# Optimization experiments

Hardware: AMD Instinct MI355X
Metric: run time of the kernel (lower is better)

The kernel has to match this reference:

```python
import jax, jax.numpy as jnp
import numpy as np

EPS = 1e-5
N_NODES = 50000


def batchnorm(x, gamma, beta):
    # training-mode BatchNorm1d: batch mean, biased variance
    mean = jnp.mean(x, axis=0)
    var = jnp.mean(jnp.square(x - mean), axis=0)
    return (x - mean) * jax.lax.rsqrt(var + EPS) * gamma + beta


def setup_inputs() -> dict:
    key = jax.random.key(0)
    ks = jax.random.split(key, 8)
    N, E, D_IN, D_H, D_OUT = N_NODES, 800000, 128, 128, 128
    feat = jax.random.normal(ks[0], (N, D_IN), dtype=jnp.float32)
    w = jax.random.uniform(ks[1], (E,), dtype=jnp.float32)
    # xavier_uniform with relu gain for Q and W
    gain = float(np.sqrt(2.0))
    bq = gain * np.sqrt(6.0 / (D_IN + D_H))
    bw = gain * np.sqrt(6.0 / (D_IN + D_H + D_OUT))
    Q_w = jax.random.uniform(ks[2], (D_H, D_IN), minval=-bq, maxval=bq, dtype=jnp.float32)
    W_w = jax.random.uniform(ks[3], (D_OUT, D_IN + D_H), minval=-bw, maxval=bw, dtype=jnp.float32)
    Q_b = jnp.zeros((D_H,), jnp.float32)
    W_b = jnp.zeros((D_OUT,), jnp.float32)
    gamma2 = jnp.ones((D_OUT,), jnp.float32)
    beta2 = jnp.zeros((D_OUT,), jnp.float32)
    src = jax.random.randint(ks[4], (E,), 0, N, dtype=jnp.int32)
    dst = jax.random.randint(ks[5], (E,), 0, N, dtype=jnp.int32)
    return {"feat": feat, "w": w, "Q_w": Q_w, "Q_b": Q_b, "W_w": W_w,
            "W_b": W_b, "gamma2": gamma2, "beta2": beta2, "src": src, "dst": dst}


def reference(feat, w, Q_w, Q_b, W_w, W_b, gamma2, beta2, src, dst):
    N = feat.shape[0]
    # h = dropout(bnorm_two(relu(Q(feat))))  (dropout=0 -> identity; source reuses bnorm_two)
    h = batchnorm(jax.nn.relu(feat @ Q_w.T + Q_b), gamma2, beta2)  # [N, H]
    # weighted neighbor mean: sum_e w_e * h[src_e] scattered to dst, / sum_e w_e
    num = jax.ops.segment_sum(w[:, None] * h[src], dst, num_segments=N)  # [N, H]
    den = jax.ops.segment_sum(w, dst, num_segments=N)  # [N]
    has_msg = den[:, None] != 0
    agg = jnp.where(has_msg, num / jnp.where(has_msg, den[:, None], 1.0), h)
    rst = jnp.concatenate([feat, agg], axis=1) @ W_w.T + W_b  # [N, OUT]
    rst = batchnorm(jax.nn.relu(rst), gamma2, beta2)
    denom = jnp.linalg.norm(rst, axis=1, keepdims=True)
    return rst / jnp.where(denom == 0, 1.0, denom)
```

## Files before the change

### kernel.cpp

```cpp
#include <hip/hip_runtime.h>
#include <stdint.h>


#define BN_EPS 1e-5f
#define NSLOT 32

typedef __attribute__((ext_vector_type(8))) short bf16x8;
typedef __attribute__((ext_vector_type(4))) float f32x4;

static __device__ __forceinline__ unsigned short f2bf(float f) {
    uint32_t u = __builtin_bit_cast(uint32_t, f);
    u += 0x7fffu + ((u >> 16) & 1u);
    return (unsigned short)(u >> 16);
}
static __device__ __forceinline__ float bf_lo(uint32_t u) {
    return __builtin_bit_cast(float, u << 16);
}
static __device__ __forceinline__ float bf_hi(uint32_t u) {
    return __builtin_bit_cast(float, u & 0xffff0000u);
}

static __device__ __forceinline__ void cast_blk(
    const float* __restrict__ src, unsigned short* __restrict__ dst,
    int n, int blk)
{
    int i = (blk * 256 + threadIdx.x) * 4;
    if (i + 3 < n) {
        float4 v = *(const float4*)(src + i);
        ushort4 o;
        o.x = f2bf(v.x); o.y = f2bf(v.y); o.z = f2bf(v.z); o.w = f2bf(v.w);
        *(ushort4*)(dst + i) = o;
    } else {
        for (int j = i; j < n; ++j) dst[j] = f2bf(src[j]);
    }
}

__global__ __launch_bounds__(256) void k_pre(
    const float* __restrict__ feat, unsigned short* __restrict__ featb, int nf,
    const int* __restrict__ dst, int* __restrict__ ccnt, int E, int CB, int HB,
    const float* __restrict__ Qw, unsigned short* __restrict__ Qwb,
    const float* __restrict__ Ww, unsigned short* __restrict__ Wwb)
{
    int b = (int)blockIdx.x;
    if (b < CB) { cast_blk(feat, featb, nf, b); return; }
    b -= CB;
    if (b >= HB) {
        b -= HB;
        if (b < 16) cast_blk(Qw, Qwb, 128 * 128, b);
        else        cast_blk(Ww, Wwb, 128 * 256, b - 16);
        return;
    }
    __shared__ int hcnt[128];
    const int tid = threadIdx.x;
    if (tid < 128) hcnt[tid] = 0;
    __syncthreads();
    const int base_e = b * 2048;
#pragma unroll
    for (int j = 0; j < 8; ++j) {
        int e = base_e + j * 256 + tid;
        if (e < E) atomicAdd(&hcnt[dst[e] >> 9], 1);
    }
    __syncthreads();
    if (tid < 128 && hcnt[tid] > 0) atomicAdd(&ccnt[tid], hcnt[tid]);
}

__global__ __launch_bounds__(128) void k_coffs(
    const int* __restrict__ ccnt, int* __restrict__ coffs,
    int* __restrict__ gcur, int* __restrict__ offs, int N, int E)
{
    __shared__ int w0sum;
    const int t = threadIdx.x;
    const int lane = t & 63, wv = t >> 6;
    int v = ccnt[t];
    int incl = v;
#pragma unroll
    for (int o = 1; o < 64; o <<= 1) {
        int u = __shfl_up(incl, o, 64);
        if (lane >= o) incl += u;
    }
    if (wv == 0 && lane == 63) w0sum = incl;
    __syncthreads();
    int excl = incl - v + (wv ? w0sum : 0);
    coffs[t] = excl;
    gcur[t]  = excl;
    if (t == 127) { coffs[128] = excl + v; offs[N] = E; }
}

template<int K, bool OUT_BF16>
static __device__ __forceinline__ void gemm_body(
    int bid,
    const unsigned short* __restrict__ A_lo,
    const unsigned short* __restrict__ A_hi,
    const unsigned short* __restrict__ Bb,
    const float* __restrict__ bias,
    void* __restrict__ Yv,
    double* __restrict__ sum, double* __restrict__ sumsq, int N)
{
    constexpr int SA = 72;
    __shared__ unsigned short As[64 * SA];
    __shared__ unsigned short Bs[128 * SA];
    __shared__ float bsum_s[128], bsq_s[128];

    const int tid  = threadIdx.x;
    const int lane = tid & 63;
    const int wv   = tid >> 6;
    const int wr   = wv >> 1;
    const int wc   = wv & 1;
    const int m15  = lane & 15;
    const int quad = lane >> 4;
    const int r0   = bid * 64;

    if (tid < 128) { bsum_s[tid] = 0.f; bsq_s[tid] = 0.f; }

    f32x4 acc[2][4];
#pragma unroll
    for (int rt = 0; rt < 2; ++rt)
#pragma unroll
        for (int ct = 0; ct < 4; ++ct)
            acc[rt][ct] = (f32x4){0.f, 0.f, 0.f, 0.f};

    for (int kc = 0; kc < K; kc += 64) {
        const unsigned short* Ap = (kc < 128) ? A_lo : A_hi;
        const int koff = kc & 127;
#pragma unroll
        for (int i = 0; i < 2; ++i) {
            int idx = i * 256 + tid;
            int row = idx >> 3, seg = idx & 7;
            int gr  = r0 + row; if (gr >= N) gr = N - 1;
            uint4 v = *(const uint4*)(Ap + (size_t)gr * 128 + koff + seg * 8);
            *(uint4*)(As + row * SA + seg * 8) = v;
        }
#pragma unroll
        for (int i = 0; i < 4; ++i) {
            int idx = i * 256 + tid;
            int row = idx >> 3, seg = idx & 7;
            uint4 v = *(const uint4*)(Bb + (size_t)row * K + kc + seg * 8);
            *(uint4*)(Bs + row * SA + seg * 8) = v;
        }
        __syncthreads();

#pragma unroll
        for (int ks = 0; ks < 64; ks += 32) {
            bf16x8 af[2], bfr[4];
#pragma unroll
            for (int rt = 0; rt < 2; ++rt)
                af[rt] = *(const bf16x8*)(As + (wr * 32 + rt * 16 + m15) * SA + ks + quad * 8);
#pragma unroll
            for (int ct = 0; ct < 4; ++ct)
                bfr[ct] = *(const bf16x8*)(Bs + (wc * 64 + ct * 16 + m15) * SA + ks + quad * 8);
#pragma unroll
            for (int rt = 0; rt < 2; ++rt)
#pragma unroll
                for (int ct = 0; ct < 4; ++ct)
                    acc[rt][ct] = __builtin_amdgcn_mfma_f32_16x16x32_bf16(
                        af[rt], bfr[ct], acc[rt][ct], 0, 0, 0);
        }
        __syncthreads();
    }

#pragma unroll
    for (int ct = 0; ct < 4; ++ct) {
        int col = wc * 64 + ct * 16 + m15;
        float bz = bias[col];
        float s = 0.f, q = 0.f;
#pragma unroll
        for (int rt = 0; rt < 2; ++rt) {
#pragma unroll
            for (int reg = 0; reg < 4; ++reg) {
                int row = r0 + wr * 32 + rt * 16 + quad * 4 + reg;
                float vv = fmaxf(acc[rt][ct][reg] + bz, 0.f);
                if (row < N) {
                    if constexpr (OUT_BF16)
                        ((unsigned short*)Yv)[(size_t)row * 128 + col] = f2bf(vv);
                    else
                        ((float*)Yv)[(size_t)row * 128 + col] = vv;
                } else {
                    vv = 0.f;
                }
                s += vv; q = fmaf(vv, vv, q);
            }
        }
        s += __shfl_xor(s, 16, 64); s += __shfl_xor(s, 32, 64);
        q += __shfl_xor(q, 16, 64); q += __shfl_xor(q, 32, 64);
        if (quad == 0) {
            atomicAdd(&bsum_s[col], s);
            atomicAdd(&bsq_s[col], q);
        }
    }
    __syncthreads();
    if (tid < 128) {
        const int slot = (bid & (NSLOT - 1)) * 128;
        atomicAdd(&sum[slot + tid],   (double)bsum_s[tid]);
        atomicAdd(&sumsq[slot + tid], (double)bsq_s[tid]);
    }
}

static __device__ __forceinline__ void bn_coef_body(
    int t, const double* __restrict__ sum, const double* __restrict__ sumsq,
    const float* __restrict__ gamma, const float* __restrict__ beta,
    float* __restrict__ a, float* __restrict__ b, double invN)
{
    double ms = 0.0, qs = 0.0;
#pragma unroll
    for (int s = 0; s < NSLOT; ++s) {
        ms += sum[s * 128 + t];
        qs += sumsq[s * 128 + t];
    }
    float mean = (float)(ms * invN);
    float var  = (float)(qs * invN) - mean * mean;
    float sc = rsqrtf(var + BN_EPS) * gamma[t];
    a[t] = sc;
    b[t] = fmaf(-mean, sc, beta[t]);
}

__global__ __launch_bounds__(128) void bn_coef(
    const double* __restrict__ sum, const double* __restrict__ sumsq,
    const float* __restrict__ gamma, const float* __restrict__ beta,
    float* __restrict__ a, float* __restrict__ b, double invN)
{
    bn_coef_body(threadIdx.x, sum, sumsq, gamma, beta, a, b, invN);
}

static __device__ __forceinline__ void bin_body(
    int bid,
    const int* __restrict__ src, const int* __restrict__ dst,
    const float* __restrict__ w, int* __restrict__ gcur,
    int4* __restrict__ tmp, int E)
{
    __shared__ int hcnt[128];
    __shared__ int hbase[128];
    const int tid = threadIdx.x;
    if (tid < 128) hcnt[tid] = 0;
    __syncthreads();

    int d8[8], s8[8], slot8[8];
    float w8[8];
#pragma unroll
    for (int j = 0; j < 8; ++j) {
        int e = bid * 2048 + j * 256 + tid;
        if (e < E) {
            d8[j] = dst[e]; s8[j] = src[e]; w8[j] = w[e];
            slot8[j] = atomicAdd(&hcnt[d8[j] >> 9], 1);
        } else d8[j] = -1;
    }
    __syncthreads();
    if (tid < 128 && hcnt[tid] > 0)
        hbase[tid] = atomicAdd(&gcur[tid], hcnt[tid]);
    __syncthreads();
#pragma unroll
    for (int j = 0; j < 8; ++j) {
        if (d8[j] >= 0) {
            int pos = hbase[d8[j] >> 9] + slot8[j];
            tmp[pos] = make_int4(s8[j], __float_as_int(w8[j]), d8[j], 0);
        }
    }
}

__global__ __launch_bounds__(256) void k_bin_gemm(
    const int* __restrict__ src, const int* __restrict__ dst,
    const float* __restrict__ w, int* __restrict__ gcur,
    int4* __restrict__ tmp, int E, int HB,
    const unsigned short* __restrict__ featb,
    const unsigned short* __restrict__ Qwb, const float* __restrict__ Qb,
    unsigned short* __restrict__ y1b,
    double* __restrict__ sum, double* __restrict__ sumsq, int N)
{
    if ((int)blockIdx.x < HB)
        bin_body(blockIdx.x, src, dst, w, gcur, tmp, E);
    else
        gemm_body<128, true>(blockIdx.x - HB, featb, featb, Qwb, Qb, y1b,
                             sum, sumsq, N);
}

static __device__ __forceinline__ void refine_body(
    int b,
    const int4* __restrict__ tmp, const int* __restrict__ coffs,
    int* __restrict__ offs, int2* __restrict__ epack, int N)
{
    __shared__ int hist[512];
    __shared__ int wpre[4];
    const int d0   = b << 9;
    const int dlim = min(512, N - d0);
    const int tid  = threadIdx.x;
    const int lane = tid & 63, wv = tid >> 6;
    const int start = coffs[b];
    const int end   = coffs[b + 1];

    hist[tid] = 0; hist[tid + 256] = 0;
    __syncthreads();

    for (int p = start + tid; p < end; p += 256)
        atomicAdd(&hist[tmp[p].z - d0], 1);
    __syncthreads();

    int v0 = hist[2 * tid], v1 = hist[2 * tid + 1];
    int s = v0 + v1;
    int incl = s;
#pragma unroll
    for (int o = 1; o < 64; o <<= 1) {
        int t = __shfl_up(incl, o, 64);
        if (lane >= o) incl += t;
    }
    if (lane == 63) wpre[wv] = incl;
    __syncthreads();
    if (tid == 0) {
        int r = 0;
#pragma unroll
        for (int i = 0; i < 4; ++i) { int t = wpre[i]; wpre[i] = r; r += t; }
    }
    __syncthreads();
    int e0 = start + wpre[wv] + incl - s;
    if (2 * tid < dlim)     offs[d0 + 2 * tid]     = e0;
    if (2 * tid + 1 < dlim) offs[d0 + 2 * tid + 1] = e0 + v0;
    hist[2 * tid]     = e0;
    hist[2 * tid + 1] = e0 + v0;
    __syncthreads();

    for (int p = start + tid; p < end; p += 256) {
        int4 rec = tmp[p];
        int pos = atomicAdd(&hist[rec.z - d0], 1);
        epack[pos] = make_int2(rec.x, rec.y);
    }
}

__global__ __launch_bounds__(256) void k_bnref(
    const double* __restrict__ sum, const double* __restrict__ sumsq,
    const float* __restrict__ gamma, const float* __restrict__ beta,
    float* __restrict__ a, float* __restrict__ b, double invN,
    const int4* __restrict__ tmp, const int* __restrict__ coffs,
    int* __restrict__ offs, int2* __restrict__ epack, int N)
{
    if (blockIdx.x == 0) {
        if (threadIdx.x < 128)
            bn_coef_body(threadIdx.x, sum, sumsq, gamma, beta, a, b, invN);
        return;
    }
    refine_body((int)blockIdx.x - 1, tmp, coffs, offs, epack, N);
}

__global__ __launch_bounds__(256) void gather_agg(
    const unsigned short* __restrict__ y1b,
    const int* __restrict__ offs, const int2* __restrict__ epack,
    const float* __restrict__ a, const float* __restrict__ b,
    unsigned short* __restrict__ aggb, int N)
{
    const int r    = (int)((blockIdx.x * 256u + threadIdx.x) >> 6);
    const int lane = threadIdx.x & 63;
    const int li   = lane & 31;
    const int hf   = lane >> 5;
    if (r >= N) return;
    int p = offs[r];
    const int end = offs[r + 1];
    float ac0 = 0.f, ac1 = 0.f, ac2 = 0.f, ac3 = 0.f, den = 0.f;
    for (; p + 3 < end; p += 4) {
        int2 ea = epack[p + hf];
        int2 eb = epack[p + 2 + hf];
        uint2 ua = *(const uint2*)(y1b + (size_t)ea.x * 128 + 4 * li);
        uint2 ub = *(const uint2*)(y1b + (size_t)eb.x * 128 + 4 * li);
        float wa = __int_as_float(ea.y), wb = __int_as_float(eb.y);
        ac0 = fmaf(wa, bf_lo(ua.x), ac0); ac1 = fmaf(wa, bf_hi(ua.x), ac1);
        ac2 = fmaf(wa, bf_lo(ua.y), ac2); ac3 = fmaf(wa, bf_hi(ua.y), ac3);
        ac0 = fmaf(wb, bf_lo(ub.x), ac0); ac1 = fmaf(wb, bf_hi(ub.x), ac1);
        ac2 = fmaf(wb, bf_lo(ub.y), ac2); ac3 = fmaf(wb, bf_hi(ub.y), ac3);
        den += wa + wb;
    }
    for (; p + 1 < end; p += 2) {
        int2 ea = epack[p + hf];
        uint2 ua = *(const uint2*)(y1b + (size_t)ea.x * 128 + 4 * li);
        float wa = __int_as_float(ea.y);
        ac0 = fmaf(wa, bf_lo(ua.x), ac0); ac1 = fmaf(wa, bf_hi(ua.x), ac1);
        ac2 = fmaf(wa, bf_lo(ua.y), ac2); ac3 = fmaf(wa, bf_hi(ua.y), ac3);
        den += wa;
    }
    if (p < end && hf == 0) {
        int2 ea = epack[p];
        uint2 ua = *(const uint2*)(y1b + (size_t)ea.x * 128 + 4 * li);
        float wa = __int_as_float(ea.y);
        ac0 = fmaf(wa, bf_lo(ua.x), ac0); ac1 = fmaf(wa, bf_hi(ua.x), ac1);
        ac2 = fmaf(wa, bf_lo(ua.y), ac2); ac3 = fmaf(wa, bf_hi(ua.y), ac3);
        den += wa;
    }
    ac0 += __shfl_xor(ac0, 32, 64);
    ac1 += __shfl_xor(ac1, 32, 64);
    ac2 += __shfl_xor(ac2, 32, 64);
    ac3 += __shfl_xor(ac3, 32, 64);
    den += __shfl_xor(den, 32, 64);
    if (hf) return;
    const int c = 4 * li;
    float4 av = *(const float4*)(a + c);
    float4 bv = *(const float4*)(b + c);
    float m0, m1, m2, m3;
    if (den != 0.f) {
        float inv = 1.f / den;
        m0 = ac0 * inv; m1 = ac1 * inv; m2 = ac2 * inv; m3 = ac3 * inv;
    } else {
        uint2 u = *(const uint2*)(y1b + (size_t)r * 128 + c);
        m0 = bf_lo(u.x); m1 = bf_hi(u.x); m2 = bf_lo(u.y); m3 = bf_hi(u.y);
    }
    ushort4 o;
    o.x = f2bf(fmaf(av.x, m0, bv.x));
    o.y = f2bf(fmaf(av.y, m1, bv.y));
    o.z = f2bf(fmaf(av.z, m2, bv.z));
    o.w = f2bf(fmaf(av.w, m3, bv.w));
    *(ushort4*)(aggb + (size_t)r * 128 + c) = o;
}

__global__ __launch_bounds__(256) void gemm_bn2(
    const unsigned short* __restrict__ A_lo,
    const unsigned short* __restrict__ A_hi,
    const unsigned short* __restrict__ Bb,
    const float* __restrict__ bias,
    float* __restrict__ Y,
    double* __restrict__ sum, double* __restrict__ sumsq, int N)
{
    gemm_body<256, false>(blockIdx.x, A_lo, A_hi, Bb, bias, Y, sum, sumsq, N);
}

__global__ __launch_bounds__(256) void finalize(
    const float* __restrict__ Y2,
    const float* __restrict__ a, const float* __restrict__ b,
    float* __restrict__ out, int N)
{
    __shared__ float sa[128], sb[128];
    const int t = threadIdx.x;
    if (t < 128) { sa[t] = a[t]; sb[t] = b[t]; }
    __syncthreads();
    const int row  = (int)((blockIdx.x * 256u + t) >> 6);
    const int lane = t & 63;
    if (row >= N) return;
    const size_t base = (size_t)row * 128;
    float v0 = fmaf(sa[lane],      Y2[base + lane],      sb[lane]);
    float v1 = fmaf(sa[lane + 64], Y2[base + lane + 64], sb[lane + 64]);
    float ss = fmaf(v0, v0, v1 * v1);
#pragma unroll
    for (int o = 32; o; o >>= 1) ss += __shfl_xor(ss, o, 64);
    float nrm = sqrtf(ss);
    float inv = (nrm == 0.f) ? 1.f : 1.f / nrm;
    out[base + lane]      = v0 * inv;
    out[base + lane + 64] = v1 * inv;
}

extern "C" void kernel_launch(void* const* d_in, const int* in_sizes, int n_in,
                              void* d_out, int out_size, void* d_ws, size_t ws_size,
                              hipStream_t stream)
{
    const float* feat   = (const float*)d_in[0];
    const float* w      = (const float*)d_in[1];
    const float* Q_w    = (const float*)d_in[2];
    const float* Q_b    = (const float*)d_in[3];
    const float* W_w    = (const float*)d_in[4];
    const float* W_b    = (const float*)d_in[5];
    const float* gamma2 = (const float*)d_in[6];
    const float* beta2  = (const float*)d_in[7];
    const int*   src    = (const int*)d_in[8];
    const int*   dst    = (const int*)d_in[9];

    const int N = in_sizes[0] / 128;
    const int E = in_sizes[1];

    float*          y2    = (float*)d_ws;
    unsigned short* featb = (unsigned short*)(y2 + (size_t)N * 128);
    unsigned short* aggb  = featb + (size_t)N * 128;
    unsigned short* y1b   = aggb + (size_t)N * 128;
    int4*  tmp    = (int4*)(y1b + (size_t)N * 128);
    int2*  epack  = (int2*)(tmp + E);
    int*   offs   = (int*)(epack + E);
    int*   coffs  = offs + (N + 1);
    int*   gcur   = coffs + 129;
    float* coefs  = (float*)(gcur + 128);
    float* a1 = coefs, *b1 = coefs + 128, *a2 = coefs + 256, *b2 = coefs + 384;
    uintptr_t qp = ((uintptr_t)(coefs + 512) + 15) & ~(uintptr_t)15;
    unsigned short* Qwb = (unsigned short*)qp;
    unsigned short* Wwb = Qwb + 128 * 128;
    uintptr_t sp = ((uintptr_t)(Wwb + 128 * 256) + 15) & ~(uintptr_t)15;
    double* stats = (double*)sp;
    double* sum1   = stats;
    double* sumsq1 = stats + NSLOT * 128;
    double* sum2   = stats + 2 * NSLOT * 128;
    double* sumsq2 = stats + 3 * NSLOT * 128;
    int*   ccnt   = (int*)(stats + 4 * NSLOT * 128);

    hipMemsetAsync(stats, 0,
                   4 * NSLOT * 128 * sizeof(double) + 128 * sizeof(int),
                   stream);

    const double invN = 1.0 / (double)N;
    const int GB = (N + 63) / 64;
    const int NB = (N + 511) >> 9;
    const int CB = (N * 128 / 4 + 255) / 256;
    const int HB = (E + 2047) / 2048;
    const int QB = 16;
    const int WB = 32;

    k_pre<<<CB + HB + QB + WB, 256, 0, stream>>>(
        feat, featb, N * 128, dst, ccnt, E, CB, HB,
        Q_w, Qwb, W_w, Wwb);
    k_coffs<<<1, 128, 0, stream>>>(ccnt, coffs, gcur, offs, N, E);

    k_bin_gemm<<<HB + GB, 256, 0, stream>>>(
        src, dst, w, gcur, tmp, E, HB,
        featb, Qwb, Q_b, y1b, sum1, sumsq1, N);

    k_bnref<<<NB + 1, 256, 0, stream>>>(
        sum1, sumsq1, gamma2, beta2, a1, b1, invN,
        tmp, coffs, offs, epack, N);

    gather_agg<<<(N * 64 + 255) / 256, 256, 0, stream>>>(
        y1b, offs, epack, a1, b1, aggb, N);

    gemm_bn2<<<GB, 256, 0, stream>>>(
        featb, aggb, Wwb, W_b, y2, sum2, sumsq2, N);
    bn_coef<<<1, 128, 0, stream>>>(sum2, sumsq2, gamma2, beta2, a2, b2, invN);
    finalize<<<(N * 64 + 255) / 256, 256, 0, stream>>>(
        y2, a2, b2, (float*)d_out, N);
}
```

Before: 227.7 us.

## Fuse neighbor gather-aggregation into second GEMM prologue via shared memory

The separate gather_agg kernel is removed. The second GEMM block now computes the weighted neighbor mean and batchnorm affine for its 64 rows directly into shared memory, then uses that tile as the upper K half of the A operand. This avoids writing and re-reading the bf16 agg buffer and saves one kernel launch. In exchange, the gather now runs at the lower parallelism of the GEMM grid (one block per 64 rows, one wave per row at a time, serialized over 16 iterations), which can reduce latency hiding for the random gathers.

```diff
diff --git a/kernel.cpp b/kernel.cpp
--- a/kernel.cpp
+++ b/kernel.cpp
@@ -86,14 +86,12 @@
     if (t == 127) { coffs[128] = excl + v; offs[N] = E; }
 }
 
-template<int K, bool OUT_BF16>
-static __device__ __forceinline__ void gemm_body(
+static __device__ __forceinline__ void gemm1_body(
     int bid,
-    const unsigned short* __restrict__ A_lo,
-    const unsigned short* __restrict__ A_hi,
+    const unsigned short* __restrict__ A,
     const unsigned short* __restrict__ Bb,
     const float* __restrict__ bias,
-    void* __restrict__ Yv,
+    unsigned short* __restrict__ Y,
     double* __restrict__ sum, double* __restrict__ sumsq, int N)
 {
     constexpr int SA = 72;
@@ -119,22 +117,20 @@
         for (int ct = 0; ct < 4; ++ct)
             acc[rt][ct] = (f32x4){0.f, 0.f, 0.f, 0.f};
 
-    for (int kc = 0; kc < K; kc += 64) {
-        const unsigned short* Ap = (kc < 128) ? A_lo : A_hi;
-        const int koff = kc & 127;
+    for (int kc = 0; kc < 128; kc += 64) {
 #pragma unroll
         for (int i = 0; i < 2; ++i) {
             int idx = i * 256 + tid;
             int row = idx >> 3, seg = idx & 7;
             int gr  = r0 + row; if (gr >= N) gr = N - 1;
-            uint4 v = *(const uint4*)(Ap + (size_t)gr * 128 + koff + seg * 8);
+            uint4 v = *(const uint4*)(A + (size_t)gr * 128 + kc + seg * 8);
             *(uint4*)(As + row * SA + seg * 8) = v;
         }
 #pragma unroll
         for (int i = 0; i < 4; ++i) {
             int idx = i * 256 + tid;
             int row = idx >> 3, seg = idx & 7;
-            uint4 v = *(const uint4*)(Bb + (size_t)row * K + kc + seg * 8);
+            uint4 v = *(const uint4*)(Bb + (size_t)row * 128 + kc + seg * 8);
             *(uint4*)(Bs + row * SA + seg * 8) = v;
         }
         __syncthreads();
@@ -170,10 +166,7 @@
                 int row = r0 + wr * 32 + rt * 16 + quad * 4 + reg;
                 float vv = fmaxf(acc[rt][ct][reg] + bz, 0.f);
                 if (row < N) {
-                    if constexpr (OUT_BF16)
-                        ((unsigned short*)Yv)[(size_t)row * 128 + col] = f2bf(vv);
-                    else
-                        ((float*)Yv)[(size_t)row * 128 + col] = vv;
+                    Y[(size_t)row * 128 + col] = f2bf(vv);
                 } else {
                     vv = 0.f;
                 }
@@ -268,8 +261,7 @@
     if ((int)blockIdx.x < HB)
         bin_body(blockIdx.x, src, dst, w, gcur, tmp, E);
     else
-        gemm_body<128, true>(blockIdx.x - HB, featb, featb, Qwb, Qb, y1b,
-                             sum, sumsq, N);
+        gemm1_body(blockIdx.x - HB, featb, Qwb, Qb, y1b, sum, sumsq, N);
 }
 
 static __device__ __forceinline__ void refine_body(
@@ -338,82 +330,178 @@
     refine_body((int)blockIdx.x - 1, tmp, coffs, offs, epack, N);
 }
 
-__global__ __launch_bounds__(256) void gather_agg(
+__global__ __launch_bounds__(256) void gemm2_fused(
+    const unsigned short* __restrict__ featb,
     const unsigned short* __restrict__ y1b,
     const int* __restrict__ offs, const int2* __restrict__ epack,
-    const float* __restrict__ a, const float* __restrict__ b,
-    unsigned short* __restrict__ aggb, int N)
-{
-    const int r    = (int)((blockIdx.x * 256u + threadIdx.x) >> 6);
-    const int lane = threadIdx.x & 63;
-    const int li   = lane & 31;
-    const int hf   = lane >> 5;
-    if (r >= N) return;
-    int p = offs[r];
-    const int end = offs[r + 1];
-    float ac0 = 0.f, ac1 = 0.f, ac2 = 0.f, ac3 = 0.f, den = 0.f;
-    for (; p + 3 < end; p += 4) {
-        int2 ea = epack[p + hf];
-        int2 eb = epack[p + 2 + hf];
-        uint2 ua = *(const uint2*)(y1b + (size_t)ea.x * 128 + 4 * li);
-        uint2 ub = *(const uint2*)(y1b + (size_t)eb.x * 128 + 4 * li);
-        float wa = __int_as_float(ea.y), wb = __int_as_float(eb.y);
-        ac0 = fmaf(wa, bf_lo(ua.x), ac0); ac1 = fmaf(wa, bf_hi(ua.x), ac1);
-        ac2 = fmaf(wa, bf_lo(ua.y), ac2); ac3 = fmaf(wa, bf_hi(ua.y), ac3);
-        ac0 = fmaf(wb, bf_lo(ub.x), ac0); ac1 = fmaf(wb, bf_hi(ub.x), ac1);
-        ac2 = fmaf(wb, bf_lo(ub.y), ac2); ac3 = fmaf(wb, bf_hi(ub.y), ac3);
-        den += wa + wb;
-    }
-    for (; p + 1 < end; p += 2) {
-        int2 ea = epack[p + hf];
-        uint2 ua = *(const uint2*)(y1b + (size_t)ea.x * 128 + 4 * li);
-        float wa = __int_as_float(ea.y);
-        ac0 = fmaf(wa, bf_lo(ua.x), ac0); ac1 = fmaf(wa, bf_hi(ua.x), ac1);
-        ac2 = fmaf(wa, bf_lo(ua.y), ac2); ac3 = fmaf(wa, bf_hi(ua.y), ac3);
-        den += wa;
-    }
-    if (p < end && hf == 0) {
-        int2 ea = epack[p];
-        uint2 ua = *(const uint2*)(y1b + (size_t)ea.x * 128 + 4 * li);
-        float wa = __int_as_float(ea.y);
-        ac0 = fmaf(wa, bf_lo(ua.x), ac0); ac1 = fmaf(wa, bf_hi(ua.x), ac1);
-        ac2 = fmaf(wa, bf_lo(ua.y), ac2); ac3 = fmaf(wa, bf_hi(ua.y), ac3);
-        den += wa;
-    }
-    ac0 += __shfl_xor(ac0, 32, 64);
-    ac1 += __shfl_xor(ac1, 32, 64);
-    ac2 += __shfl_xor(ac2, 32, 64);
-    ac3 += __shfl_xor(ac3, 32, 64);
-    den += __shfl_xor(den, 32, 64);
-    if (hf) return;
-    const int c = 4 * li;
-    float4 av = *(const float4*)(a + c);
-    float4 bv = *(const float4*)(b + c);
-    float m0, m1, m2, m3;
-    if (den != 0.f) {
-        float inv = 1.f / den;
-        m0 = ac0 * inv; m1 = ac1 * inv; m2 = ac2 * inv; m3 = ac3 * inv;
-    } else {
-        uint2 u = *(const uint2*)(y1b + (size_t)r * 128 + c);
-        m0 = bf_lo(u.x); m1 = bf_hi(u.x); m2 = bf_lo(u.y); m3 = bf_hi(u.y);
-    }
-    ushort4 o;
-    o.x = f2bf(fmaf(av.x, m0, bv.x));
-    o.y = f2bf(fmaf(av.y, m1, bv.y));
-    o.z = f2bf(fmaf(av.z, m2, bv.z));
-    o.w = f2bf(fmaf(av.w, m3, bv.w));
-    *(ushort4*)(aggb + (size_t)r * 128 + c) = o;
-}
-
-__global__ __launch_bounds__(256) void gemm_bn2(
-    const unsigned short* __restrict__ A_lo,
-    const unsigned short* __restrict__ A_hi,
+    const float* __restrict__ a1, const float* __restrict__ b1,
     const unsigned short* __restrict__ Bb,
     const float* __restrict__ bias,
     float* __restrict__ Y,
     double* __restrict__ sum, double* __restrict__ sumsq, int N)
 {
-    gemm_body<256, false>(blockIdx.x, A_lo, A_hi, Bb, bias, Y, sum, sumsq, N);
+    constexpr int SA = 72;
+    __shared__ unsigned short As[64 * SA];
+    __shared__ unsigned short Bs[128 * SA];
+    __shared__ unsigned short Ag[2][64 * SA];
+    __shared__ float bsum_s[128], bsq_s[128];
+
+    const int tid  = threadIdx.x;
+    const int lane = tid & 63;
+    const int wv   = tid >> 6;
+    const int wr   = wv >> 1;
+    const int wc   = wv & 1;
+    const int m15  = lane & 15;
+    const int quad = lane >> 4;
+    const int r0   = (int)blockIdx.x * 64;
+
+    if (tid < 128) { bsum_s[tid] = 0.f; bsq_s[tid] = 0.f; }
+
+    const int li = lane & 31;
+    const int hf = lane >> 5;
+    const int c  = 4 * li;
+    const float4 av = *(const float4*)(a1 + c);
+    const float4 bv = *(const float4*)(b1 + c);
+#pragma unroll 1
+    for (int i = 0; i < 16; ++i) {
+        const int lr = wv + 4 * i;
+        const int r  = r0 + lr;
+        float ac0 = 0.f, ac1 = 0.f, ac2 = 0.f, ac3 = 0.f, den = 0.f;
+        if (r < N) {
+            int p = offs[r];
+            const int end = offs[r + 1];
+            for (; p + 3 < end; p += 4) {
+                int2 ea = epack[p + hf];
+                int2 eb = epack[p + 2 + hf];
+                uint2 ua = *(const uint2*)(y1b + (size_t)ea.x * 128 + c);
+                uint2 ub = *(const uint2*)(y1b + (size_t)eb.x * 128 + c);
+                float wa = __int_as_float(ea.y), wb = __int_as_float(eb.y);
+                ac0 = fmaf(wa, bf_lo(ua.x), ac0); ac1 = fmaf(wa, bf_hi(ua.x), ac1);
+                ac2 = fmaf(wa, bf_lo(ua.y), ac2); ac3 = fmaf(wa, bf_hi(ua.y), ac3);
+                ac0 = fmaf(wb, bf_lo(ub.x), ac0); ac1 = fmaf(wb, bf_hi(ub.x), ac1);
+                ac2 = fmaf(wb, bf_lo(ub.y), ac2); ac3 = fmaf(wb, bf_hi(ub.y), ac3);
+                den += wa + wb;
+            }
+            for (; p + 1 < end; p += 2) {
+                int2 ea = epack[p + hf];
+                uint2 ua = *(const uint2*)(y1b + (size_t)ea.x * 128 + c);
+                float wa = __int_as_float(ea.y);
+                ac0 = fmaf(wa, bf_lo(ua.x), ac0); ac1 = fmaf(wa, bf_hi(ua.x), ac1);
+                ac2 = fmaf(wa, bf_lo(ua.y), ac2); ac3 = fmaf(wa, bf_hi(ua.y), ac3);
+                den += wa;
+            }
+            if (p < end && hf == 0) {
+                int2 ea = epack[p];
+                uint2 ua = *(const uint2*)(y1b + (size_t)ea.x * 128 + c);
+                float wa = __int_as_float(ea.y);
+                ac0 = fmaf(wa, bf_lo(ua.x), ac0); ac1 = fmaf(wa, bf_hi(ua.x), ac1);
+                ac2 = fmaf(wa, bf_lo(ua.y), ac2); ac3 = fmaf(wa, bf_hi(ua.y), ac3);
+                den += wa;
+            }
+        }
+        ac0 += __shfl_xor(ac0, 32, 64);
+        ac1 += __shfl_xor(ac1, 32, 64);
+        ac2 += __shfl_xor(ac2, 32, 64);
+        ac3 += __shfl_xor(ac3, 32, 64);
+        den += __shfl_xor(den, 32, 64);
+        if (hf == 0) {
+            float m0 = 0.f, m1 = 0.f, m2 = 0.f, m3 = 0.f;
+            if (den != 0.f) {
+                float inv = 1.f / den;
+                m0 = ac0 * inv; m1 = ac1 * inv; m2 = ac2 * inv; m3 = ac3 * inv;
+            } else if (r < N) {
+                uint2 u = *(const uint2*)(y1b + (size_t)r * 128 + c);
+                m0 = bf_lo(u.x); m1 = bf_hi(u.x); m2 = bf_lo(u.y); m3 = bf_hi(u.y);
+            }
+            ushort4 o;
+            o.x = f2bf(fmaf(av.x, m0, bv.x));
+            o.y = f2bf(fmaf(av.y, m1, bv.y));
+            o.z = f2bf(fmaf(av.z, m2, bv.z));
+            o.w = f2bf(fmaf(av.w, m3, bv.w));
+            *(ushort4*)(Ag[li >> 4] + lr * SA + (c & 63)) = o;
+        }
+    }
+    __syncthreads();
+
+    f32x4 acc[2][4];
+#pragma unroll
+    for (int rt = 0; rt < 2; ++rt)
+#pragma unroll
+        for (int ct = 0; ct < 4; ++ct)
+            acc[rt][ct] = (f32x4){0.f, 0.f, 0.f, 0.f};
+
+    for (int kc = 0; kc < 256; kc += 64) {
+        if (kc < 128) {
+#pragma unroll
+            for (int i = 0; i < 2; ++i) {
+                int idx = i * 256 + tid;
+                int row = idx >> 3, seg = idx & 7;
+                int gr  = r0 + row; if (gr >= N) gr = N - 1;
+                uint4 v = *(const uint4*)(featb + (size_t)gr * 128 + kc + seg * 8);
+                *(uint4*)(As + row * SA + seg * 8) = v;
+            }
+        }
+#pragma unroll
+        for (int i = 0; i < 4; ++i) {
+            int idx = i * 256 + tid;
+            int row = idx >> 3, seg = idx & 7;
+            uint4 v = *(const uint4*)(Bb + (size_t)row * 256 + kc + seg * 8);
+            *(uint4*)(Bs + row * SA + seg * 8) = v;
+        }
+        __syncthreads();
+
+        const unsigned short* Ap = (kc < 128) ? As : Ag[(kc >> 6) & 1];
+#pragma unroll
+        for (int ks = 0; ks < 64; ks += 32) {
+            bf16x8 af[2], bfr[4];
+#pragma unroll
+            for (int rt = 0; rt < 2; ++rt)
+                af[rt] = *(const bf16x8*)(Ap + (wr * 32 + rt * 16 + m15) * SA + ks + quad * 8);
+#pragma unroll
+            for (int ct = 0; ct < 4; ++ct)
+                bfr[ct] = *(const bf16x8*)(Bs + (wc * 64 + ct * 16 + m15) * SA + ks + quad * 8);
+#pragma unroll
+            for (int rt = 0; rt < 2; ++rt)
+#pragma unroll
+                for (int ct = 0; ct < 4; ++ct)
+                    acc[rt][ct] = __builtin_amdgcn_mfma_f32_16x16x32_bf16(
+                        af[rt], bfr[ct], acc[rt][ct], 0, 0, 0);
+        }
+        __syncthreads();
+    }
+
+#pragma unroll
+    for (int ct = 0; ct < 4; ++ct) {
+        int col = wc * 64 + ct * 16 + m15;
+        float bz = bias[col];
+        float s = 0.f, q = 0.f;
+#pragma unroll
+        for (int rt = 0; rt < 2; ++rt) {
+#pragma unroll
+            for (int reg = 0; reg < 4; ++reg) {
+                int row = r0 + wr * 32 + rt * 16 + quad * 4 + reg;
+                float vv = fmaxf(acc[rt][ct][reg] + bz, 0.f);
+                if (row < N) {
+                    Y[(size_t)row * 128 + col] = vv;
+                } else {
+                    vv = 0.f;
+                }
+                s += vv; q = fmaf(vv, vv, q);
+            }
+        }
+        s += __shfl_xor(s, 16, 64); s += __shfl_xor(s, 32, 64);
+        q += __shfl_xor(q, 16, 64); q += __shfl_xor(q, 32, 64);
+        if (quad == 0) {
+            atomicAdd(&bsum_s[col], s);
+            atomicAdd(&bsq_s[col], q);
+        }
+    }
+    __syncthreads();
+    if (tid < 128) {
+        const int slot = ((int)blockIdx.x & (NSLOT - 1)) * 128;
+        atomicAdd(&sum[slot + tid],   (double)bsum_s[tid]);
+        atomicAdd(&sumsq[slot + tid], (double)bsq_s[tid]);
+    }
 }
 
 __global__ __launch_bounds__(256) void finalize(
@@ -460,8 +548,7 @@
 
     float*          y2    = (float*)d_ws;
     unsigned short* featb = (unsigned short*)(y2 + (size_t)N * 128);
-    unsigned short* aggb  = featb + (size_t)N * 128;
-    unsigned short* y1b   = aggb + (size_t)N * 128;
+    unsigned short* y1b   = featb + (size_t)N * 128;
     int4*  tmp    = (int4*)(y1b + (size_t)N * 128);
     int2*  epack  = (int2*)(tmp + E);
     int*   offs   = (int*)(epack + E);
@@ -505,11 +592,10 @@
         sum1, sumsq1, gamma2, beta2, a1, b1, invN,
         tmp, coffs, offs, epack, N);
 
-    gather_agg<<<(N * 64 + 255) / 256, 256, 0, stream>>>(
-        y1b, offs, epack, a1, b1, aggb, N);
-
-    gemm_bn2<<<GB, 256, 0, stream>>>(
-        featb, aggb, Wwb, W_b, y2, sum2, sumsq2, N);
+    gemm2_fused<<<GB, 256, 0, stream>>>(
+        featb, y1b, offs, epack, a1, b1, Wwb, W_b,
+        y2, sum2, sumsq2, N);
+
     bn_coef<<<1, 128, 0, stream>>>(sum2, sumsq2, gamma2, beta2, a2, b2, invN);
     finalize<<<(N * 64 + 255) / 256, 256, 0, stream>>>(
         y2, a2, b2, (float*)d_out, N);
```

Result: slower. 300.6 us (+32.0%).

## Remove coarse-offset scan kernel by recomputing scan in consumers; unroll gather by 8

Applied to the files above, without the earlier changes.

Drops the single-block k_coffs launch. The bin and refine blocks now each redo the 128-entry prefix scan of the bucket counts, and bin blocks add the scanned base to a zero-initialised per-bucket cursor. The offs[N] sentinel write moves into k_pre. Separately, the gather loop gains an 8-edge unrolled step to keep more independent row loads in flight. The cost is a redundant small scan in every bin and refine block, plus more registers in the gather.

```diff
diff --git a/kernel.cpp b/kernel.cpp
--- a/kernel.cpp
+++ b/kernel.cpp
@@ -35,14 +35,42 @@
     }
 }
 
+static __device__ __forceinline__ void scan_ccnt(
+    const int* __restrict__ ccnt, int* excl_out, int* v_out, int* w0s)
+{
+    const int t = threadIdx.x;
+    int v = 0, incl = 0;
+    if (t < 128) {
+        v = ccnt[t];
+        incl = v;
+        const int lane = t & 63;
+#pragma unroll
+        for (int o = 1; o < 64; o <<= 1) {
+            int u = __shfl_up(incl, o, 64);
+            if (lane >= o) incl += u;
+        }
+        if (t == 63) *w0s = incl;
+    }
+    __syncthreads();
+    int excl = 0;
+    if (t < 128) excl = incl - v + ((t >> 6) ? *w0s : 0);
+    *excl_out = excl;
+    *v_out = v;
+}
+
 __global__ __launch_bounds__(256) void k_pre(
     const float* __restrict__ feat, unsigned short* __restrict__ featb, int nf,
     const int* __restrict__ dst, int* __restrict__ ccnt, int E, int CB, int HB,
     const float* __restrict__ Qw, unsigned short* __restrict__ Qwb,
-    const float* __restrict__ Ww, unsigned short* __restrict__ Wwb)
+    const float* __restrict__ Ww, unsigned short* __restrict__ Wwb,
+    int* __restrict__ offs, int N)
 {
     int b = (int)blockIdx.x;
-    if (b < CB) { cast_blk(feat, featb, nf, b); return; }
+    if (b < CB) {
+        if (b == 0 && threadIdx.x == 0) offs[N] = E;
+        cast_blk(feat, featb, nf, b);
+        return;
+    }
     b -= CB;
     if (b >= HB) {
         b -= HB;
@@ -62,28 +90,6 @@
     }
     __syncthreads();
     if (tid < 128 && hcnt[tid] > 0) atomicAdd(&ccnt[tid], hcnt[tid]);
-}
-
-__global__ __launch_bounds__(128) void k_coffs(
-    const int* __restrict__ ccnt, int* __restrict__ coffs,
-    int* __restrict__ gcur, int* __restrict__ offs, int N, int E)
-{
-    __shared__ int w0sum;
-    const int t = threadIdx.x;
-    const int lane = t & 63, wv = t >> 6;
-    int v = ccnt[t];
-    int incl = v;
-#pragma unroll
-    for (int o = 1; o < 64; o <<= 1) {
-        int u = __shfl_up(incl, o, 64);
-        if (lane >= o) incl += u;
-    }
-    if (wv == 0 && lane == 63) w0sum = incl;
-    __syncthreads();
-    int excl = incl - v + (wv ? w0sum : 0);
-    coffs[t] = excl;
-    gcur[t]  = excl;
-    if (t == 127) { coffs[128] = excl + v; offs[N] = E; }
 }
 
 template<int K, bool OUT_BF16>
@@ -224,11 +230,13 @@
 static __device__ __forceinline__ void bin_body(
     int bid,
     const int* __restrict__ src, const int* __restrict__ dst,
-    const float* __restrict__ w, int* __restrict__ gcur,
+    const float* __restrict__ w,
+    const int* __restrict__ ccnt, int* __restrict__ gofs,
     int4* __restrict__ tmp, int E)
 {
     __shared__ int hcnt[128];
     __shared__ int hbase[128];
+    __shared__ int w0s;
     const int tid = threadIdx.x;
     if (tid < 128) hcnt[tid] = 0;
     __syncthreads();
@@ -244,8 +252,10 @@
         } else d8[j] = -1;
     }
     __syncthreads();
+    int excl, vcnt;
+    scan_ccnt(ccnt, &excl, &vcnt, &w0s);
     if (tid < 128 && hcnt[tid] > 0)
-        hbase[tid] = atomicAdd(&gcur[tid], hcnt[tid]);
+        hbase[tid] = excl + atomicAdd(&gofs[tid], hcnt[tid]);
     __syncthreads();
 #pragma unroll
     for (int j = 0; j < 8; ++j) {
@@ -258,7 +268,8 @@
 
 __global__ __launch_bounds__(256) void k_bin_gemm(
     const int* __restrict__ src, const int* __restrict__ dst,
-    const float* __restrict__ w, int* __restrict__ gcur,
+    const float* __restrict__ w,
+    const int* __restrict__ ccnt, int* __restrict__ gofs,
     int4* __restrict__ tmp, int E, int HB,
     const unsigned short* __restrict__ featb,
     const unsigned short* __restrict__ Qwb, const float* __restrict__ Qb,
@@ -266,7 +277,7 @@
     double* __restrict__ sum, double* __restrict__ sumsq, int N)
 {
     if ((int)blockIdx.x < HB)
-        bin_body(blockIdx.x, src, dst, w, gcur, tmp, E);
+        bin_body(blockIdx.x, src, dst, w, ccnt, gofs, tmp, E);
     else
         gemm_body<128, true>(blockIdx.x - HB, featb, featb, Qwb, Qb, y1b,
                              sum, sumsq, N);
@@ -274,20 +285,26 @@
 
 static __device__ __forceinline__ void refine_body(
     int b,
-    const int4* __restrict__ tmp, const int* __restrict__ coffs,
+    const int4* __restrict__ tmp, const int* __restrict__ ccnt,
     int* __restrict__ offs, int2* __restrict__ epack, int N)
 {
     __shared__ int hist[512];
     __shared__ int wpre[4];
+    __shared__ int w0s;
+    __shared__ int sbounds[2];
     const int d0   = b << 9;
     const int dlim = min(512, N - d0);
     const int tid  = threadIdx.x;
     const int lane = tid & 63, wv = tid >> 6;
-    const int start = coffs[b];
-    const int end   = coffs[b + 1];
 
     hist[tid] = 0; hist[tid + 256] = 0;
     __syncthreads();
+    int excl, vcnt;
+    scan_ccnt(ccnt, &excl, &vcnt, &w0s);
+    if (tid == b) { sbounds[0] = excl; sbounds[1] = excl + vcnt; }
+    __syncthreads();
+    const int start = sbounds[0];
+    const int end   = sbounds[1];
 
     for (int p = start + tid; p < end; p += 256)
         atomicAdd(&hist[tmp[p].z - d0], 1);
@@ -327,7 +344,7 @@
     const double* __restrict__ sum, const double* __restrict__ sumsq,
     const float* __restrict__ gamma, const float* __restrict__ beta,
     float* __restrict__ a, float* __restrict__ b, double invN,
-    const int4* __restrict__ tmp, const int* __restrict__ coffs,
+    const int4* __restrict__ tmp, const int* __restrict__ ccnt,
     int* __restrict__ offs, int2* __restrict__ epack, int N)
 {
     if (blockIdx.x == 0) {
@@ -335,7 +352,7 @@
             bn_coef_body(threadIdx.x, sum, sumsq, gamma, beta, a, b, invN);
         return;
     }
-    refine_body((int)blockIdx.x - 1, tmp, coffs, offs, epack, N);
+    refine_body((int)blockIdx.x - 1, tmp, ccnt, offs, epack, N);
 }
 
 __global__ __launch_bounds__(256) void gather_agg(
@@ -351,12 +368,34 @@
     if (r >= N) return;
     int p = offs[r];
     const int end = offs[r + 1];
+    const int c = 4 * li;
     float ac0 = 0.f, ac1 = 0.f, ac2 = 0.f, ac3 = 0.f, den = 0.f;
+    for (; p + 7 < end; p += 8) {
+        int2 e0 = epack[p + hf];
+        int2 e1 = epack[p + 2 + hf];
+        int2 e2 = epack[p + 4 + hf];
+        int2 e3 = epack[p + 6 + hf];
+        uint2 u0 = *(const uint2*)(y1b + (size_t)e0.x * 128 + c);
+        uint2 u1 = *(const uint2*)(y1b + (size_t)e1.x * 128 + c);
+        uint2 u2 = *(const uint2*)(y1b + (size_t)e2.x * 128 + c);
+        uint2 u3 = *(const uint2*)(y1b + (size_t)e3.x * 128 + c);
+        float w0 = __int_as_float(e0.y), w1 = __int_as_float(e1.y);
+        float w2 = __int_as_float(e2.y), w3 = __int_as_float(e3.y);
+        ac0 = fmaf(w0, bf_lo(u0.x), ac0); ac1 = fmaf(w0, bf_hi(u0.x), ac1);
+        ac2 = fmaf(w0, bf_lo(u0.y), ac2); ac3 = fmaf(w0, bf_hi(u0.y), ac3);
+        ac0 = fmaf(w1, bf_lo(u1.x), ac0); ac1 = fmaf(w1, bf_hi(u1.x), ac1);
+        ac2 = fmaf(w1, bf_lo(u1.y), ac2); ac3 = fmaf(w1, bf_hi(u1.y), ac3);
+        ac0 = fmaf(w2, bf_lo(u2.x), ac0); ac1 = fmaf(w2, bf_hi(u2.x), ac1);
+        ac2 = fmaf(w2, bf_lo(u2.y), ac2); ac3 = fmaf(w2, bf_hi(u2.y), ac3);
+        ac0 = fmaf(w3, bf_lo(u3.x), ac0); ac1 = fmaf(w3, bf_hi(u3.x), ac1);
+        ac2 = fmaf(w3, bf_lo(u3.y), ac2); ac3 = fmaf(w3, bf_hi(u3.y), ac3);
+        den += (w0 + w1) + (w2 + w3);
+    }
     for (; p + 3 < end; p += 4) {
         int2 ea = epack[p + hf];
         int2 eb = epack[p + 2 + hf];
-        uint2 ua = *(const uint2*)(y1b + (size_t)ea.x * 128 + 4 * li);
-        uint2 ub = *(const uint2*)(y1b + (size_t)eb.x * 128 + 4 * li);
+        uint2 ua = *(const uint2*)(y1b + (size_t)ea.x * 128 + c);
+        uint2 ub = *(const uint2*)(y1b + (size_t)eb.x * 128 + c);
         float wa = __int_as_float(ea.y), wb = __int_as_float(eb.y);
         ac0 = fmaf(wa, bf_lo(ua.x), ac0); ac1 = fmaf(wa, bf_hi(ua.x), ac1);
         ac2 = fmaf(wa, bf_lo(ua.y), ac2); ac3 = fmaf(wa, bf_hi(ua.y), ac3);
@@ -366,7 +405,7 @@
     }
     for (; p + 1 < end; p += 2) {
         int2 ea = epack[p + hf];
-        uint2 ua = *(const uint2*)(y1b + (size_t)ea.x * 128 + 4 * li);
+        uint2 ua = *(const uint2*)(y1b + (size_t)ea.x * 128 + c);
         float wa = __int_as_float(ea.y);
         ac0 = fmaf(wa, bf_lo(ua.x), ac0); ac1 = fmaf(wa, bf_hi(ua.x), ac1);
         ac2 = fmaf(wa, bf_lo(ua.y), ac2); ac3 = fmaf(wa, bf_hi(ua.y), ac3);
@@ -374,7 +413,7 @@
     }
     if (p < end && hf == 0) {
         int2 ea = epack[p];
-        uint2 ua = *(const uint2*)(y1b + (size_t)ea.x * 128 + 4 * li);
+        uint2 ua = *(const uint2*)(y1b + (size_t)ea.x * 128 + c);
         float wa = __int_as_float(ea.y);
         ac0 = fmaf(wa, bf_lo(ua.x), ac0); ac1 = fmaf(wa, bf_hi(ua.x), ac1);
         ac2 = fmaf(wa, bf_lo(ua.y), ac2); ac3 = fmaf(wa, bf_hi(ua.y), ac3);
@@ -386,7 +425,6 @@
     ac3 += __shfl_xor(ac3, 32, 64);
     den += __shfl_xor(den, 32, 64);
     if (hf) return;
-    const int c = 4 * li;
     float4 av = *(const float4*)(a + c);
     float4 bv = *(const float4*)(b + c);
     float m0, m1, m2, m3;
@@ -465,9 +503,7 @@
     int4*  tmp    = (int4*)(y1b + (size_t)N * 128);
     int2*  epack  = (int2*)(tmp + E);
     int*   offs   = (int*)(epack + E);
-    int*   coffs  = offs + (N + 1);
-    int*   gcur   = coffs + 129;
-    float* coefs  = (float*)(gcur + 128);
+    float* coefs  = (float*)(offs + N + 1);
     float* a1 = coefs, *b1 = coefs + 128, *a2 = coefs + 256, *b2 = coefs + 384;
     uintptr_t qp = ((uintptr_t)(coefs + 512) + 15) & ~(uintptr_t)15;
     unsigned short* Qwb = (unsigned short*)qp;
@@ -479,9 +515,10 @@
     double* sum2   = stats + 2 * NSLOT * 128;
     double* sumsq2 = stats + 3 * NSLOT * 128;
     int*   ccnt   = (int*)(stats + 4 * NSLOT * 128);
+    int*   gofs   = ccnt + 128;
 
     hipMemsetAsync(stats, 0,
-                   4 * NSLOT * 128 * sizeof(double) + 128 * sizeof(int),
+                   4 * NSLOT * 128 * sizeof(double) + 256 * sizeof(int),
                    stream);
 
     const double invN = 1.0 / (double)N;
@@ -494,22 +531,22 @@
 
     k_pre<<<CB + HB + QB + WB, 256, 0, stream>>>(
         feat, featb, N * 128, dst, ccnt, E, CB, HB,
-        Q_w, Qwb, W_w, Wwb);
-    k_coffs<<<1, 128, 0, stream>>>(ccnt, coffs, gcur, offs, N, E);
+        Q_w, Qwb, W_w, Wwb, offs, N);
 
     k_bin_gemm<<<HB + GB, 256, 0, stream>>>(
-        src, dst, w, gcur, tmp, E, HB,
+        src, dst, w, ccnt, gofs, tmp, E, HB,
         featb, Qwb, Q_b, y1b, sum1, sumsq1, N);
 
     k_bnref<<<NB + 1, 256, 0, stream>>>(
         sum1, sumsq1, gamma2, beta2, a1, b1, invN,
-        tmp, coffs, offs, epack, N);
+        tmp, ccnt, offs, epack, N);
 
     gather_agg<<<(N * 64 + 255) / 256, 256, 0, stream>>>(
         y1b, offs, epack, a1, b1, aggb, N);
 
     gemm_bn2<<<GB, 256, 0, stream>>>(
         featb, aggb, Wwb, W_b, y2, sum2, sumsq2, N);
+
     bn_coef<<<1, 128, 0, stream>>>(sum2, sumsq2, gamma2, beta2, a2, b2, invN);
     finalize<<<(N * 64 + 255) / 256, 256, 0, stream>>>(
         y2, a2, b2, (float*)d_out, N);
```

New measurement: 225.8 us. About the same (-0.8%).
